# Kernel optimization log

Measured on AMD Instinct MI355X. Metric: run time of the kernel, lower is better.

## Reference

```python
import jax, jax.numpy as jnp
import numpy as np

N = 100000   # num_nodes
E = 1600000  # num_edges (avg degree 16)
D = 64       # embed_channels
C = 16       # num_classes
EPSILON = 0.1  # AntiSymmetricConv step size (PyG default)
GAMMA = 0.1    # AntiSymmetricConv diffusion strength (PyG default)


def setup_inputs() -> dict:
    key = jax.random.key(0)
    ks = jax.random.split(key, 9)
    s = 1.0 / np.sqrt(D)
    return {
        "edge_index": jax.random.randint(ks[0], (2, E), 0, N, dtype=jnp.int32),
        "embed_w": jax.random.normal(ks[1], (N, D), dtype=jnp.float32) * 0.1,
        "W_rel": jax.random.normal(ks[2], (D, D), dtype=jnp.float32) * s,   # GraphConv lin_rel weight
        "b_rel": jax.random.normal(ks[3], (D,), dtype=jnp.float32) * s,     # GraphConv lin_rel bias
        "W_root": jax.random.normal(ks[4], (D, D), dtype=jnp.float32) * s,  # GraphConv lin_root weight (no bias)
        "W_anti": jax.random.normal(ks[5], (D, D), dtype=jnp.float32) * s,  # AntiSymmetricConv W
        "b_anti": jax.random.normal(ks[6], (D,), dtype=jnp.float32) * s,    # AntiSymmetricConv bias
        "W_lin": jax.random.normal(ks[7], (C, D), dtype=jnp.float32) * s,   # lin2 weight
        "b_lin": jax.random.normal(ks[8], (C,), dtype=jnp.float32) * s,     # lin2 bias
    }


def reference(edge_index, embed_w, W_rel, b_rel, W_root, W_anti, b_anti, W_lin, b_lin):
    x = embed_w  # [N, D] node features = embedding table
    src, dst = edge_index[0], edge_index[1]
    # phi = GraphConv with 'add' aggregation: lin_rel(sum_j x_j) + lin_root(x)
    agg = jax.ops.segment_sum(x[src], dst, num_segments=N)  # [N, D] sparse gather+scatter-add
    h = agg @ W_rel.T + b_rel + x @ W_root.T
    # antisymmetric weight: W - W^T - gamma * I
    aW = W_anti - W_anti.T - GAMMA * jnp.eye(D, dtype=x.dtype)
    h = x @ aW.T + h + b_anti
    h = jnp.tanh(h)                       # default act of AntiSymmetricConv
    x = x + EPSILON * h                   # single iteration (num_iters=1 default)
    # dropout p=0.0 -> identity
    out = jax.nn.sigmoid(x @ W_lin.T + b_lin)  # [N, C]
    return out
```

## Files before the change

### kernel.cpp

```cpp
#include <hip/hip_runtime.h>

#define DD 64
#define CC 16
#define EPSILON 0.1f
#define GAMMA 0.1f
#define BSH 6
#define BSZ 64
#define CAP 1280
#define MAXBK 2048
#define PAD 65
#define PADW 65
#define CSH 10
#define MAXNC 128
#define CPAD 16
#define CAPC 20480
#define L1CHUNK 2048
#define L1THR 512
#define NSLICE 8

typedef float v2f __attribute__((ext_vector_type(2)));

__global__ __launch_bounds__(L1THR) void bin_coarse_conv(
        const int* __restrict__ ei, int* __restrict__ gcntc,
        unsigned* __restrict__ binned_c, int E,
        const float* __restrict__ x, unsigned* __restrict__ x_q, int N,
        const float* __restrict__ Wrel, const float* __restrict__ Wroot,
        const float* __restrict__ Wanti, const float* __restrict__ brel,
        const float* __restrict__ banti,
        float* __restrict__ B_g, float* __restrict__ bc) {
    __shared__ int hist[MAXNC], gbase[MAXNC], cur[MAXNC];
    const int t = threadIdx.x;
    if (t < MAXNC) { hist[t] = 0; cur[t] = 0; }
    __syncthreads();
    const int e0 = blockIdx.x * L1CHUNK;
    int srcv[4], dstv[4];
    const int e = e0 + 4 * t;
    if (e + 4 <= E) {
        int4 s4 = *(const int4*)&ei[e];
        int4 d4 = *(const int4*)&ei[E + e];
        srcv[0] = s4.x; srcv[1] = s4.y; srcv[2] = s4.z; srcv[3] = s4.w;
        dstv[0] = d4.x; dstv[1] = d4.y; dstv[2] = d4.z; dstv[3] = d4.w;
    } else {
#pragma unroll
        for (int i = 0; i < 4; ++i) {
            if (e + i < E) { srcv[i] = ei[e + i]; dstv[i] = ei[E + e + i]; }
            else dstv[i] = -1;
        }
    }
#pragma unroll
    for (int i = 0; i < 4; ++i)
        if (dstv[i] >= 0) atomicAdd(&hist[dstv[i] >> CSH], 1);
    __syncthreads();
    if (t < MAXNC) {
        int h = hist[t];
        gbase[t] = h ? atomicAdd(&gcntc[t * CPAD], h) : 0;
    }
    __syncthreads();
#pragma unroll
    for (int i = 0; i < 4; ++i) {
        if (dstv[i] >= 0) {
            int b = dstv[i] >> CSH;
            int pos = gbase[b] + atomicAdd(&cur[b], 1);
            if (pos < CAPC)
                binned_c[(size_t)b * CAPC + pos] =
                    (unsigned)srcv[i] |
                    ((unsigned)(dstv[i] & ((1 << CSH) - 1)) << 17);
        }
    }
    if (blockIdx.x == 0) {
        for (int idx = t; idx < 128 * 64; idx += L1THR) {
            int k = idx >> 6, d = idx & 63;
            float v;
            if (k < 64) {
                v = Wrel[d * 64 + k];
            } else {
                int j = k - 64;
                v = Wroot[d * 64 + j] + Wanti[d * 64 + j] - Wanti[j * 64 + d];
                if (d == j) v -= GAMMA;
            }
            B_g[idx] = v;
        }
        if (t < 64) bc[t] = brel[t] + banti[t];
    }
    const float4* x4 = (const float4*)x;
    const int M = N * (DD / 4);
    const int G = gridDim.x * L1THR;
    for (int i = blockIdx.x * L1THR + t; i < M; i += G) {
        float4 a = x4[i];
        int r = __builtin_amdgcn_cvt_pk_fp8_f32(a.x, a.y, 0, false);
        r = __builtin_amdgcn_cvt_pk_fp8_f32(a.z, a.w, r, true);
        x_q[i] = (unsigned)r;
    }
}

__global__ __launch_bounds__(256) void bin_fine(
        const int* __restrict__ gcntc, const unsigned* __restrict__ binned_c,
        int* __restrict__ gcnt, unsigned* __restrict__ binned) {
    __shared__ int hist[16];
    __shared__ int hbase[16];
    const int t = threadIdx.x;
    const int c = blockIdx.x >> 3, s = blockIdx.x & (NSLICE - 1);
    int cnt = gcntc[c * CPAD];
    if (cnt > CAPC) cnt = CAPC;
    const int per = (cnt + NSLICE - 1) / NSLICE;
    const int i0 = s * per;
    int i1 = i0 + per;
    if (i1 > cnt) i1 = cnt;
    if (t < 16) hist[t] = 0;
    __syncthreads();
    const unsigned* bcp = binned_c + (size_t)c * CAPC;
    unsigned ent[10];
#pragma unroll
    for (int j = 0; j < 10; ++j) {
        int i = i0 + t + j * 256;
        ent[j] = (i < i1) ? bcp[i] : 0xFFFFFFFFu;
        if (ent[j] != 0xFFFFFFFFu) atomicAdd(&hist[ent[j] >> (17 + BSH)], 1);
    }
    __syncthreads();
    if (t < 16) {
        hbase[t] = hist[t] ? atomicAdd(&gcnt[c * 16 + t], hist[t]) : 0;
        hist[t] = 0;
    }
    __syncthreads();
#pragma unroll
    for (int j = 0; j < 10; ++j) {
        if (ent[j] != 0xFFFFFFFFu) {
            unsigned dstc = ent[j] >> 17;
            int f = dstc >> BSH;
            int pos = hbase[f] + atomicAdd(&hist[f], 1);
            if (pos < CAP)
                binned[(size_t)(c * 16 + f) * CAP + pos] =
                    (ent[j] & 0x1FFFF) | ((dstc & (BSZ - 1)) << 17);
        }
    }
}

__global__ __launch_bounds__(512, 8) void mega(
        const float* __restrict__ x, const unsigned* __restrict__ x_q,
        const int* __restrict__ gcnt, const unsigned* __restrict__ binned,
        const float* __restrict__ B_g, const float* __restrict__ bc,
        const float* __restrict__ Wlin, const float* __restrict__ blin,
        float* __restrict__ out, int N) {
    __shared__ float R0[BSZ * PAD];
    __shared__ float wl_sh[CC * PADW];
    __shared__ int csr[CAP];
    __shared__ int deg[BSZ], offs[BSZ], cur[BSZ];

    const int t = threadIdx.x;
    const int b = blockIdx.x;
    const int nb0 = b << BSH;
    int cnt = gcnt[b];
    if (cnt > CAP) cnt = CAP;
    const unsigned* bl = binned + (size_t)b * CAP;

#pragma unroll
    for (int i = 0; i < 2; ++i) {
        int idx = t + 512 * i;
        wl_sh[(idx >> 6) * PADW + (idx & 63)] = Wlin[idx];
    }
    if (t < BSZ) deg[t] = 0;
    __syncthreads();
    for (int i = t; i < cnt; i += 512) atomicAdd(&deg[bl[i] >> 17], 1);
    __syncthreads();
    if (t < BSZ) offs[t] = deg[t];
    __syncthreads();
    for (int off = 1; off < BSZ; off <<= 1) {
        int v = 0;
        if (t < BSZ && t >= off) v = offs[t - off];
        __syncthreads();
        if (t < BSZ) offs[t] += v;
        __syncthreads();
    }
    if (t < BSZ) {
        int ex = offs[t] - deg[t];
        offs[t] = ex;
        cur[t] = ex;
    }
    __syncthreads();
    for (int i = t; i < cnt; i += 512) {
        unsigned en = bl[i];
        int pos = atomicAdd(&cur[en >> 17], 1);
        csr[pos] = (int)(en & 0x1FFFF);
    }
    __syncthreads();

    {
        const int g = t >> 3, q = t & 7;
        const uint2* xq2 = (const uint2*)x_q;
        const int i0 = offs[g], dc = deg[g];
        float a[8];
#pragma unroll
        for (int r = 0; r < 8; ++r) a[r] = 0.f;
        int i = 0;
        for (; i + 8 <= dc; i += 8) {
            int s0 = csr[i0 + i + 0], s1 = csr[i0 + i + 1];
            int s2 = csr[i0 + i + 2], s3 = csr[i0 + i + 3];
            int s4 = csr[i0 + i + 4], s5 = csr[i0 + i + 5];
            int s6 = csr[i0 + i + 6], s7 = csr[i0 + i + 7];
            uint2 v0 = xq2[s0 * 8 + q];
            uint2 v1 = xq2[s1 * 8 + q];
            uint2 v2 = xq2[s2 * 8 + q];
            uint2 v3 = xq2[s3 * 8 + q];
            uint2 v4 = xq2[s4 * 8 + q];
            uint2 v5 = xq2[s5 * 8 + q];
            uint2 v6 = xq2[s6 * 8 + q];
            uint2 v7 = xq2[s7 * 8 + q];
            v2f f;
#define ACC8(v)                                                               \
            f = __builtin_amdgcn_cvt_pk_f32_fp8((v).x, false); a[0] += f.x; a[1] += f.y; \
            f = __builtin_amdgcn_cvt_pk_f32_fp8((v).x, true);  a[2] += f.x; a[3] += f.y; \
            f = __builtin_amdgcn_cvt_pk_f32_fp8((v).y, false); a[4] += f.x; a[5] += f.y; \
            f = __builtin_amdgcn_cvt_pk_f32_fp8((v).y, true);  a[6] += f.x; a[7] += f.y;
            ACC8(v0); ACC8(v1); ACC8(v2); ACC8(v3);
            ACC8(v4); ACC8(v5); ACC8(v6); ACC8(v7);
        }
        for (; i < dc; ++i) {
            int s0 = csr[i0 + i];
            uint2 v0 = xq2[s0 * 8 + q];
            v2f f;
            ACC8(v0);
#undef ACC8
        }
        float* row = &R0[g * PAD + 8 * q];
#pragma unroll
        for (int r = 0; r < 8; ++r) row[r] = a[r];
    }
    __syncthreads();

    const int nl = t & 63;
    const int dg = __builtin_amdgcn_readfirstlane(t >> 6);
    float acc[8];
#pragma unroll
    for (int j = 0; j < 8; ++j) acc[j] = 0.f;
#pragma unroll 8
    for (int k = 0; k < DD; ++k) {
        float a = R0[nl * PAD + k];
        const float* Bk = &B_g[k * DD + dg * 8];
#pragma unroll
        for (int j = 0; j < 8; ++j) acc[j] = fmaf(a, Bk[j], acc[j]);
    }
    __syncthreads();

    {
        int nn = N - nb0;
        if (nn > BSZ) nn = BSZ;
        const float4* x4 = (const float4*)x;
        for (int idx = t; idx < nn * 16; idx += 512) {
            float4 v = x4[nb0 * 16 + idx];
            float* row = &R0[(idx >> 4) * PAD + (idx & 15) * 4];
            row[0] = v.x; row[1] = v.y; row[2] = v.z; row[3] = v.w;
        }
    }
    __syncthreads();

#pragma unroll 8
    for (int k = 0; k < DD; ++k) {
        float a = R0[nl * PAD + k];
        const float* Bk = &B_g[(DD + k) * DD + dg * 8];
#pragma unroll
        for (int j = 0; j < 8; ++j) acc[j] = fmaf(a, Bk[j], acc[j]);
    }

#pragma unroll
    for (int j = 0; j < 8; ++j) {
        int d = dg * 8 + j;
        float h = acc[j] + bc[d];
        float e2 = __expf(2.0f * h);
        float th = 1.0f - 2.0f / (e2 + 1.0f);
        acc[j] = R0[nl * PAD + d] + EPSILON * th;
    }
    __syncthreads();
#pragma unroll
    for (int j = 0; j < 8; ++j) R0[nl * PAD + dg * 8 + j] = acc[j];
    __syncthreads();

    {
        const int g = t >> 3, q = t & 7;
        const int n = nb0 + g;
        if (n < N) {
            float p0 = blin[2 * q], p1 = blin[2 * q + 1];
#pragma unroll 8
            for (int d = 0; d < DD; ++d) {
                float xv = R0[g * PAD + d];
                p0 = fmaf(xv, wl_sh[(2 * q) * PADW + d], p0);
                p1 = fmaf(xv, wl_sh[(2 * q + 1) * PADW + d], p1);
            }
            float2 o;
            o.x = 1.0f / (1.0f + __expf(-p0));
            o.y = 1.0f / (1.0f + __expf(-p1));
            *(float2*)(out + (size_t)n * CC + 2 * q) = o;
        }
    }
}

extern "C" void kernel_launch(void* const* d_in, const int* in_sizes, int n_in,
                              void* d_out, int out_size, void* d_ws, size_t ws_size,
                              hipStream_t stream) {
    const int*   ei    = (const int*)d_in[0];
    const float* x     = (const float*)d_in[1];
    const float* Wrel  = (const float*)d_in[2];
    const float* brel  = (const float*)d_in[3];
    const float* Wroot = (const float*)d_in[4];
    const float* Wanti = (const float*)d_in[5];
    const float* banti = (const float*)d_in[6];
    const float* Wlin  = (const float*)d_in[7];
    const float* blin  = (const float*)d_in[8];
    float* out = (float*)d_out;

    const int E = in_sizes[0] / 2;
    const int N = in_sizes[1] / DD;
    const int NC = (N + (1 << CSH) - 1) >> CSH;

    unsigned* x_q = (unsigned*)d_ws;
    unsigned* binned_c = x_q + (size_t)N * (DD / 4);
    unsigned* binned = binned_c + (size_t)MAXNC * CAPC;
    int*   gcntc = (int*)(binned + (size_t)MAXBK * CAP);
    int*   gcnt  = gcntc + MAXNC * CPAD;
    float* B_g   = (float*)(gcnt + MAXBK);
    float* bc    = B_g + 128 * 64;

    hipMemsetAsync(gcntc, 0, (MAXNC * CPAD + MAXBK) * sizeof(int), stream);
    bin_coarse_conv<<<(E + L1CHUNK - 1) / L1CHUNK, L1THR, 0, stream>>>(
        ei, gcntc, binned_c, E, x, x_q, N,
        Wrel, Wroot, Wanti, brel, banti, B_g, bc);
    bin_fine<<<NC * NSLICE, 256, 0, stream>>>(gcntc, binned_c, gcnt, binned);
    mega<<<NC * 16, 512, 0, stream>>>(x, x_q, gcnt, binned, B_g, bc, Wlin, blin,
                                      out, N);
}
```

Before: 177.1 us.

## Use bf16 MFMA for fused GEMM, prepacked B fragments, wave-shuffle scan

Replaces the scalar FMA loops for the two 64x64 GEMMs in the mega kernel with bf16 MFMA 16x16x32 instructions. The weight matrix is prepacked into fragment order in bf16 by the binning kernel, and activations are converted from LDS on the fly. It also swaps the LDS-based prefix scan for a wavefront shuffle scan and changes PAD to 68 for aligned vector LDS loads. This cuts ALU and LDS instruction count but lowers precision to bf16 and reduces the occupancy hint.

```diff
diff --git a/kernel.cpp b/kernel.cpp
--- a/kernel.cpp
+++ b/kernel.cpp
@@ -8,7 +8,7 @@
 #define BSZ 64
 #define CAP 1280
 #define MAXBK 2048
-#define PAD 65
+#define PAD 68
 #define PADW 65
 #define CSH 10
 #define MAXNC 128
@@ -19,6 +19,14 @@
 #define NSLICE 8
 
 typedef float v2f __attribute__((ext_vector_type(2)));
+typedef __attribute__((ext_vector_type(8))) short short8v;
+typedef __attribute__((ext_vector_type(4))) float f32x4;
+
+static __device__ inline short f2bf(float f) {
+    unsigned u = __builtin_bit_cast(unsigned, f);
+    unsigned r = (u + 0x7FFFu + ((u >> 16) & 1u)) >> 16;
+    return (short)r;
+}
 
 __global__ __launch_bounds__(L1THR) void bin_coarse_conv(
         const int* __restrict__ ei, int* __restrict__ gcntc,
@@ -27,7 +35,7 @@
         const float* __restrict__ Wrel, const float* __restrict__ Wroot,
         const float* __restrict__ Wanti, const float* __restrict__ brel,
         const float* __restrict__ banti,
-        float* __restrict__ B_g, float* __restrict__ bc) {
+        unsigned short* __restrict__ Bp, float* __restrict__ bc) {
     __shared__ int hist[MAXNC], gbase[MAXNC], cur[MAXNC];
     const int t = threadIdx.x;
     if (t < MAXNC) { hist[t] = 0; cur[t] = 0; }
@@ -68,17 +76,20 @@
         }
     }
     if (blockIdx.x == 0) {
-        for (int idx = t; idx < 128 * 64; idx += L1THR) {
-            int k = idx >> 6, d = idx & 63;
+        for (int idx = t; idx < 16 * 64 * 8; idx += L1THR) {
+            int j = idx & 7, l = (idx >> 3) & 63;
+            int nt = (idx >> 9) & 3, ks = idx >> 11;
+            int k = ks * 32 + ((l >> 4) << 3) + j;
+            int d = nt * 16 + (l & 15);
             float v;
             if (k < 64) {
                 v = Wrel[d * 64 + k];
             } else {
-                int j = k - 64;
-                v = Wroot[d * 64 + j] + Wanti[d * 64 + j] - Wanti[j * 64 + d];
-                if (d == j) v -= GAMMA;
+                int j2 = k - 64;
+                v = Wroot[d * 64 + j2] + Wanti[d * 64 + j2] - Wanti[j2 * 64 + d];
+                if (d == j2) v -= GAMMA;
             }
-            B_g[idx] = v;
+            Bp[idx] = (unsigned short)f2bf(v);
         }
         if (t < 64) bc[t] = brel[t] + banti[t];
     }
@@ -135,10 +146,10 @@
     }
 }
 
-__global__ __launch_bounds__(512, 8) void mega(
+__global__ __launch_bounds__(512, 6) void mega(
         const float* __restrict__ x, const unsigned* __restrict__ x_q,
         const int* __restrict__ gcnt, const unsigned* __restrict__ binned,
-        const float* __restrict__ B_g, const float* __restrict__ bc,
+        const unsigned short* __restrict__ Bp, const float* __restrict__ bc,
         const float* __restrict__ Wlin, const float* __restrict__ blin,
         float* __restrict__ out, int N) {
     __shared__ float R0[BSZ * PAD];
@@ -162,19 +173,15 @@
     __syncthreads();
     for (int i = t; i < cnt; i += 512) atomicAdd(&deg[bl[i] >> 17], 1);
     __syncthreads();
-    if (t < BSZ) offs[t] = deg[t];
-    __syncthreads();
-    for (int off = 1; off < BSZ; off <<= 1) {
-        int v = 0;
-        if (t < BSZ && t >= off) v = offs[t - off];
-        __syncthreads();
-        if (t < BSZ) offs[t] += v;
-        __syncthreads();
-    }
-    if (t < BSZ) {
-        int ex = offs[t] - deg[t];
-        offs[t] = ex;
-        cur[t] = ex;
+    if (t < 64) {
+        int v = deg[t];
+#pragma unroll
+        for (int off = 1; off < 64; off <<= 1) {
+            int u = __shfl_up(v, off, 64);
+            if (t >= off) v += u;
+        }
+        offs[t] = v - deg[t];
+        cur[t] = v - deg[t];
     }
     __syncthreads();
     for (int i = t; i < cnt; i += 512) {
@@ -227,17 +234,33 @@
     }
     __syncthreads();
 
-    const int nl = t & 63;
-    const int dg = __builtin_amdgcn_readfirstlane(t >> 6);
-    float acc[8];
-#pragma unroll
-    for (int j = 0; j < 8; ++j) acc[j] = 0.f;
-#pragma unroll 8
-    for (int k = 0; k < DD; ++k) {
-        float a = R0[nl * PAD + k];
-        const float* Bk = &B_g[k * DD + dg * 8];
-#pragma unroll
-        for (int j = 0; j < 8; ++j) acc[j] = fmaf(a, Bk[j], acc[j]);
+    const int lane = t & 63;
+    const int w = t >> 6;
+    const int nt = w & 3, mbase = (w >> 2) * 32;
+    const int arow = (mbase + (lane & 15)) * PAD + ((lane >> 4) << 3);
+    f32x4 acc0 = {0.f, 0.f, 0.f, 0.f}, acc1 = {0.f, 0.f, 0.f, 0.f};
+
+#define LDFRAG(dst, p) do {                                                   \
+        float4 u_ = *(const float4*)(p);                                      \
+        float4 v_ = *(const float4*)((p) + 4);                                \
+        dst[0] = f2bf(u_.x); dst[1] = f2bf(u_.y);                             \
+        dst[2] = f2bf(u_.z); dst[3] = f2bf(u_.w);                             \
+        dst[4] = f2bf(v_.x); dst[5] = f2bf(v_.y);                             \
+        dst[6] = f2bf(v_.z); dst[7] = f2bf(v_.w);                             \
+    } while (0)
+
+    {
+        short8v b0 = *(const short8v*)&Bp[((0 * 4 + nt) * 64 + lane) * 8];
+        short8v b1 = *(const short8v*)&Bp[((1 * 4 + nt) * 64 + lane) * 8];
+        short8v a00, a01, a10, a11;
+        LDFRAG(a00, &R0[arow]);
+        LDFRAG(a01, &R0[arow + 32]);
+        LDFRAG(a10, &R0[arow + 16 * PAD]);
+        LDFRAG(a11, &R0[arow + 16 * PAD + 32]);
+        acc0 = __builtin_amdgcn_mfma_f32_16x16x32_bf16(a00, b0, acc0, 0, 0, 0);
+        acc1 = __builtin_amdgcn_mfma_f32_16x16x32_bf16(a10, b0, acc1, 0, 0, 0);
+        acc0 = __builtin_amdgcn_mfma_f32_16x16x32_bf16(a01, b1, acc0, 0, 0, 0);
+        acc1 = __builtin_amdgcn_mfma_f32_16x16x32_bf16(a11, b1, acc1, 0, 0, 0);
     }
     __syncthreads();
 
@@ -253,25 +276,39 @@
     }
     __syncthreads();
 
-#pragma unroll 8
-    for (int k = 0; k < DD; ++k) {
-        float a = R0[nl * PAD + k];
-        const float* Bk = &B_g[(DD + k) * DD + dg * 8];
-#pragma unroll
-        for (int j = 0; j < 8; ++j) acc[j] = fmaf(a, Bk[j], acc[j]);
-    }
-
-#pragma unroll
-    for (int j = 0; j < 8; ++j) {
-        int d = dg * 8 + j;
-        float h = acc[j] + bc[d];
-        float e2 = __expf(2.0f * h);
-        float th = 1.0f - 2.0f / (e2 + 1.0f);
-        acc[j] = R0[nl * PAD + d] + EPSILON * th;
-    }
-    __syncthreads();
-#pragma unroll
-    for (int j = 0; j < 8; ++j) R0[nl * PAD + dg * 8 + j] = acc[j];
+    {
+        short8v b2 = *(const short8v*)&Bp[((2 * 4 + nt) * 64 + lane) * 8];
+        short8v b3 = *(const short8v*)&Bp[((3 * 4 + nt) * 64 + lane) * 8];
+        short8v a00, a01, a10, a11;
+        LDFRAG(a00, &R0[arow]);
+        LDFRAG(a01, &R0[arow + 32]);
+        LDFRAG(a10, &R0[arow + 16 * PAD]);
+        LDFRAG(a11, &R0[arow + 16 * PAD + 32]);
+        acc0 = __builtin_amdgcn_mfma_f32_16x16x32_bf16(a00, b2, acc0, 0, 0, 0);
+        acc1 = __builtin_amdgcn_mfma_f32_16x16x32_bf16(a10, b2, acc1, 0, 0, 0);
+        acc0 = __builtin_amdgcn_mfma_f32_16x16x32_bf16(a01, b3, acc0, 0, 0, 0);
+        acc1 = __builtin_amdgcn_mfma_f32_16x16x32_bf16(a11, b3, acc1, 0, 0, 0);
+    }
+#undef LDFRAG
+    __syncthreads();
+
+    {
+        const int dcol = nt * 16 + (lane & 15);
+        const float bcv = bc[dcol];
+#pragma unroll
+        for (int mt = 0; mt < 2; ++mt) {
+            f32x4 A = mt ? acc1 : acc0;
+#pragma unroll
+            for (int r = 0; r < 4; ++r) {
+                int nloc = mbase + mt * 16 + ((lane >> 4) << 2) + r;
+                float h = A[r] + bcv;
+                float e2 = __expf(2.0f * h);
+                float th = 1.0f - 2.0f / (e2 + 1.0f);
+                float xv = R0[nloc * PAD + dcol];
+                R0[nloc * PAD + dcol] = xv + EPSILON * th;
+            }
+        }
+    }
     __syncthreads();
 
     {
@@ -316,14 +353,14 @@
     unsigned* binned = binned_c + (size_t)MAXNC * CAPC;
     int*   gcntc = (int*)(binned + (size_t)MAXBK * CAP);
     int*   gcnt  = gcntc + MAXNC * CPAD;
-    float* B_g   = (float*)(gcnt + MAXBK);
-    float* bc    = B_g + 128 * 64;
+    unsigned short* Bp = (unsigned short*)(gcnt + MAXBK);
+    float* bc    = (float*)(Bp + 16 * 64 * 8);
 
     hipMemsetAsync(gcntc, 0, (MAXNC * CPAD + MAXBK) * sizeof(int), stream);
     bin_coarse_conv<<<(E + L1CHUNK - 1) / L1CHUNK, L1THR, 0, stream>>>(
         ei, gcntc, binned_c, E, x, x_q, N,
-        Wrel, Wroot, Wanti, brel, banti, B_g, bc);
+        Wrel, Wroot, Wanti, brel, banti, Bp, bc);
     bin_fine<<<NC * NSLICE, 256, 0, stream>>>(gcntc, binned_c, gcnt, binned);
-    mega<<<NC * 16, 512, 0, stream>>>(x, x_q, gcnt, binned, B_g, bc, Wlin, blin,
+    mega<<<NC * 16, 512, 0, stream>>>(x, x_q, gcnt, binned, Bp, bc, Wlin, blin,
                                       out, N);
 }
```

Measured after the change: 161.6 us. -8.8%, faster.
